# Kernel optimization log

Hardware: AMD Instinct MI355X
Metric: run time of the kernel (lower is better)

The kernel has to match this reference:

```python
import jax, jax.numpy as jnp
import numpy as np

N = 50000        # nodes
E = 1600000      # edges (before self loops)
IN = 128         # in_channels
HID = 32         # hidden_channels
HEADS = 4
OUT = 16         # out_channels
B = 512          # graphs in batch
NEG_SLOPE = 0.2  # PyG GATConv default


def _uniform(key, shape, fan_in):
    s = 1.0 / np.sqrt(fan_in)
    return jax.random.uniform(key, shape, jnp.float32, -s, s)


def setup_inputs() -> dict:
    key = jax.random.key(0)
    ks = jax.random.split(key, 12)
    x = jax.random.normal(ks[0], (N, IN), jnp.float32)
    edge_index = jax.random.randint(ks[1], (2, E), 0, N, dtype=jnp.int64)
    batch = jnp.sort(jax.random.randint(ks[2], (N,), 0, B, dtype=jnp.int64))
    return {
        "x": x,
        "edge_index": edge_index,
        "batch": batch,
        "W1": _uniform(ks[3], (IN, HEADS * HID), IN),
        "att_src": _uniform(ks[4], (HEADS, HID), HID),
        "att_dst": _uniform(ks[5], (HEADS, HID), HID),
        "b1": jnp.zeros((HEADS * HID,), jnp.float32),
        "lin1_w": _uniform(ks[6], (HEADS * HID, HID), HEADS * HID),
        "lin1_b": _uniform(ks[7], (HID,), HEADS * HID),
        "lin2_w": _uniform(ks[8], (HID, OUT), HID),
        "lin2_b": _uniform(ks[9], (OUT,), HID),
    }


def _gat_conv(x, src, dst, W1, att_src, att_dst, b1):
    # h: [N, H, C]
    h = (x @ W1).reshape(N, HEADS, HID)
    a_s = (h * att_src).sum(-1)   # [N, H]
    a_d = (h * att_dst).sum(-1)   # [N, H]
    # per-edge attention logits [E', H]
    alpha = jax.nn.leaky_relu(a_s[src] + a_d[dst], negative_slope=NEG_SLOPE)
    # segment softmax over incoming edges of each destination node
    amax = jax.lax.stop_gradient(jax.ops.segment_max(alpha, dst, num_segments=N))
    ex = jnp.exp(alpha - amax[dst])
    den = jax.ops.segment_sum(ex, dst, num_segments=N)
    a = ex / (den[dst] + 1e-16)
    # weighted scatter-aggregate of source features: [N, H, C]
    out = jax.ops.segment_sum(h[src] * a[:, :, None], dst, num_segments=N)
    return out.reshape(N, HEADS * HID) + b1


def reference(x, edge_index, batch, W1, att_src, att_dst, b1, lin1_w, lin1_b, lin2_w, lin2_b):
    # add self loops (PyG GATConv default add_self_loops=True)
    loop = jnp.arange(N, dtype=edge_index.dtype)
    src = jnp.concatenate([edge_index[0], loop])
    dst = jnp.concatenate([edge_index[1], loop])
    # dropout layers are identity in eval mode
    xh = jax.nn.elu(_gat_conv(x, src, dst, W1, att_src, att_dst, b1))
    g = jax.ops.segment_sum(xh, batch, num_segments=B)  # global_add_pool -> [B, H*C]
    g = g @ lin1_w + lin1_b
    return g @ lin2_w + lin2_b
```

## Files before the change

kernel.cpp:

```cpp
#include <hip/hip_runtime.h>
#include <hip/hip_bf16.h>
#include <hip/hip_fp16.h>

#define N_NODES 50000
#define E_EDGES 1600000
#define IN_CH 128
#define HID 32
#define HEADS 4
#define HC (HEADS * HID)
#define OUT_CH 16
#define B_GRAPHS 512
#define NEG_SLOPE 0.2f
#define CAP 96
#define NB 512
#define BNODES 98
#define PCAP 3584
#define ACHUNK 4096
#define APART 391
#define ROWS_PB 64
#define GEMM_BLOCKS 782
#define TOT_BLOCKS 1173

__device__ __forceinline__ unsigned short f2bf(float f) {
    unsigned int u = __float_as_uint(f);
    unsigned int r = (u + 0x7FFFu + ((u >> 16) & 1u)) >> 16;
    return (unsigned short)r;
}

__device__ __forceinline__ float lrelu_exp(float v) {
    v = v > 0.f ? v : NEG_SLOPE * v;
    return __expf(v);
}

__global__ __launch_bounds__(256) void k_fused(const float* __restrict__ x,
                                               const float* __restrict__ W1,
                                               const float* __restrict__ att_src,
                                               const float* __restrict__ att_dst,
                                               const int* __restrict__ ei,
                                               unsigned short* __restrict__ hb,
                                               float* __restrict__ a_s,
                                               float* __restrict__ a_d,
                                               int* __restrict__ gcur,
                                               unsigned int* __restrict__ ebuf,
                                               float* __restrict__ g) {
    __shared__ float smem[12288];
    const int t = threadIdx.x;
    const int bI = blockIdx.x;

    if (bI % 3 == 0) {
        const int ablk = bI / 3;
        int* scnt = (int*)smem;
        int* sbase = scnt + 4 * NB;
        const int wv = t >> 6;
        const int e0 = ablk * ACHUNK;
        int e1 = e0 + ACHUNK; if (e1 > E_EDGES) e1 = E_EDGES;
        for (int i = t; i < 4 * NB; i += 256) scnt[i] = 0;
        __syncthreads();
        const int* __restrict__ dstp = ei + E_EDGES;
        for (int e = e0 + t; e < e1; e += 256) {
            int d = dstp[e];
            atomicAdd(&scnt[wv * NB + d / BNODES], 1);
        }
        __syncthreads();
        for (int i = t; i < NB; i += 256) {
            int c0 = scnt[0 * NB + i], c1 = scnt[1 * NB + i];
            int c2 = scnt[2 * NB + i], c3 = scnt[3 * NB + i];
            int base = atomicAdd(&gcur[i], c0 + c1 + c2 + c3);
            sbase[0 * NB + i] = base;
            sbase[1 * NB + i] = base + c0;
            sbase[2 * NB + i] = base + c0 + c1;
            sbase[3 * NB + i] = base + c0 + c1 + c2;
            scnt[0 * NB + i] = 0; scnt[1 * NB + i] = 0;
            scnt[2 * NB + i] = 0; scnt[3 * NB + i] = 0;
        }
        __syncthreads();
        for (int e = e0 + t; e < e1; e += 256) {
            int d = dstp[e];
            int s = ei[e];
            int b = d / BNODES;
            int dl = d - b * BNODES;
            int pos = sbase[wv * NB + b] + atomicAdd(&scnt[wv * NB + b], 1);
            if (pos < PCAP)
                ebuf[(size_t)b * PCAP + pos] = ((unsigned int)dl << 16) | (unsigned int)s;
        }
        return;
    }

    float* sX = smem;
    float* sW = smem + 8192;
    const int bid = bI - bI / 3 - 1;
    const int n0 = bid * ROWS_PB;

    int gt = bid * 256 + t;
    if (gt < B_GRAPHS * HC) g[gt] = 0.f;

    for (int i = t; i < ROWS_PB * 32; i += 256) {
        int r = i >> 5, c4 = i & 31;
        int n = n0 + r;
        float4 v = (n < N_NODES) ? ((const float4*)x)[(size_t)n * 32 + c4]
                                 : make_float4(0.f, 0.f, 0.f, 0.f);
        ((float4*)sX)[i] = v;
    }

    float acc[8][4];
#pragma unroll
    for (int j = 0; j < 8; j++)
#pragma unroll
        for (int c = 0; c < 4; c++) acc[j][c] = 0.f;

    const int tx = t & 31;
    const int ty = t >> 5;

    for (int kb = 0; kb < 4; kb++) {
        __syncthreads();
        for (int i = t; i < 32 * 32; i += 256) {
            ((float4*)sW)[i] =
                ((const float4*)W1)[(size_t)(kb * 32 + (i >> 5)) * 32 + (i & 31)];
        }
        __syncthreads();
#pragma unroll
        for (int kk = 0; kk < 32; kk += 4) {
            float4 w0 = *(float4*)&sW[(kk + 0) * 128 + tx * 4];
            float4 w1 = *(float4*)&sW[(kk + 1) * 128 + tx * 4];
            float4 w2 = *(float4*)&sW[(kk + 2) * 128 + tx * 4];
            float4 w3 = *(float4*)&sW[(kk + 3) * 128 + tx * 4];
#pragma unroll
            for (int j = 0; j < 8; j++) {
                float4 xv = *(float4*)&sX[(ty * 8 + j) * 128 + kb * 32 + kk];
                acc[j][0] += xv.x * w0.x + xv.y * w1.x + xv.z * w2.x + xv.w * w3.x;
                acc[j][1] += xv.x * w0.y + xv.y * w1.y + xv.z * w2.y + xv.w * w3.y;
                acc[j][2] += xv.x * w0.z + xv.y * w1.z + xv.z * w2.z + xv.w * w3.z;
                acc[j][3] += xv.x * w0.w + xv.y * w1.w + xv.z * w2.w + xv.w * w3.w;
            }
        }
    }

#pragma unroll
    for (int j = 0; j < 8; j++) {
        int n = n0 + ty * 8 + j;
        if (n < N_NODES) {
            ushort4 o;
            o.x = f2bf(acc[j][0]); o.y = f2bf(acc[j][1]);
            o.z = f2bf(acc[j][2]); o.w = f2bf(acc[j][3]);
            *(ushort4*)&hb[(size_t)n * HC + tx * 4] = o;
        }
    }

    __syncthreads();
    float* sH = smem;
#pragma unroll
    for (int j = 0; j < 8; j++) {
        float* row = &sH[(ty * 8 + j) * 129 + tx * 4];
        row[0] = acc[j][0]; row[1] = acc[j][1];
        row[2] = acc[j][2]; row[3] = acc[j][3];
    }
    __syncthreads();
    if (t < 128) {
        int r = t & 63;
        int n = n0 + r;
        const float* __restrict__ av = (t < 64) ? att_src : att_dst;
        float s0 = 0.f, s1 = 0.f, s2 = 0.f, s3 = 0.f;
#pragma unroll 4
        for (int j = 0; j < 32; j++) {
            const float* row = &sH[r * 129 + j];
            s0 += row[0]  * av[j];
            s1 += row[32] * av[32 + j];
            s2 += row[64] * av[64 + j];
            s3 += row[96] * av[96 + j];
        }
        if (n < N_NODES) {
            float* dst = (t < 64) ? a_s : a_d;
            *(float4*)(dst + (size_t)n * 4) = make_float4(s0, s1, s2, s3);
        }
    }
}

#define NPW 7
__global__ __launch_bounds__(1024) void k_aggB(const unsigned int* __restrict__ ebuf,
                                               const int* __restrict__ gcur,
                                               const float* __restrict__ a_s,
                                               const float* __restrict__ a_d,
                                               const unsigned short* __restrict__ hb,
                                               const float* __restrict__ b1,
                                               const int* __restrict__ batch,
                                               float* __restrict__ g) {
    __shared__ unsigned short sbuf[BNODES * CAP];
    __shared__ int scnt[BNODES];
    __shared__ float sWt[16][4][97];
    const int t = threadIdx.x;
    const int b = blockIdx.x;
    const int dbase = b * BNODES;

    for (int i = t; i < BNODES; i += 1024) {
        int d = dbase + i;
        scnt[i] = (d < N_NODES) ? 1 : 0;
        sbuf[i * CAP] = (unsigned short)d;
    }
    __syncthreads();
    int m = gcur[b]; if (m > PCAP) m = PCAP;
    for (int i = t; i < m; i += 1024) {
        unsigned int p = ebuf[(size_t)b * PCAP + i];
        int dl = p >> 16;
        int s = p & 0xFFFFu;
        int c = atomicAdd(&scnt[dl], 1);
        if (c < CAP) sbuf[dl * CAP + c] = (unsigned short)s;
    }
    __syncthreads();

    const int wv = t >> 6;
    const int l = t & 63;
    const int head = l >> 4;
    const int c0 = 2 * l;
    int nl0 = wv * NPW;
    if (nl0 >= BNODES) return;
    int nl1 = nl0 + NPW; if (nl1 > BNODES) nl1 = BNODES;
    int gn0 = dbase + nl0;
    if (gn0 >= N_NODES) return;
    int gn1 = dbase + nl1; if (gn1 > N_NODES) gn1 = N_NODES;
    const float2 bias = *(const float2*)(b1 + c0);
    float pool0 = 0.f, pool1 = 0.f;
    int cur = batch[gn0];
    for (int n = gn0; n < gn1; n++) {
        int bb = batch[n];
        if (bb != cur) {
            atomicAdd(&g[(size_t)cur * HC + c0], pool0);
            atomicAdd(&g[(size_t)cur * HC + c0 + 1], pool1);
            pool0 = pool1 = 0.f;
            cur = bb;
        }
        int nl = n - dbase;
        int c = scnt[nl]; if (c > CAP) c = CAP;
        float4 ad = *(const float4*)(a_d + (size_t)n * 4);
        const unsigned short* __restrict__ srow = &sbuf[nl * CAP];
        for (int i = l; i < c; i += 64) {
            int s = srow[i];
            float4 as = *(const float4*)(a_s + (size_t)s * 4);
            sWt[wv][0][i] = lrelu_exp(as.x + ad.x);
            sWt[wv][1][i] = lrelu_exp(as.y + ad.y);
            sWt[wv][2][i] = lrelu_exp(as.z + ad.z);
            sWt[wv][3][i] = lrelu_exp(as.w + ad.w);
        }
        __asm__ volatile("" ::: "memory");
        const float* __restrict__ wrow = &sWt[wv][head][0];
        float acc0 = 0.f, acc1 = 0.f, dsum = 0.f;
        int i = 0;
        for (; i + 8 <= c; i += 8) {
            unsigned int u[8];
            float w[8];
#pragma unroll
            for (int q = 0; q < 8; q++) {
                int sq = srow[i + q];
                w[q] = wrow[i + q];
                u[q] = *(const unsigned int*)(hb + (size_t)sq * HC + c0);
            }
#pragma unroll
            for (int q = 0; q < 8; q++) {
                dsum += w[q];
                acc0 += w[q] * __uint_as_float(u[q] << 16);
                acc1 += w[q] * __uint_as_float(u[q] & 0xFFFF0000u);
            }
        }
        for (; i < c; i++) {
            int s0 = srow[i];
            float w0 = wrow[i];
            unsigned int u0 = *(const unsigned int*)(hb + (size_t)s0 * HC + c0);
            dsum += w0;
            acc0 += w0 * __uint_as_float(u0 << 16);
            acc1 += w0 * __uint_as_float(u0 & 0xFFFF0000u);
        }
        __asm__ volatile("" ::: "memory");
        float inv = 1.f / (dsum + 1e-16f);
        float v0 = acc0 * inv + bias.x; v0 = v0 > 0.f ? v0 : (__expf(v0) - 1.f);
        float v1 = acc1 * inv + bias.y; v1 = v1 > 0.f ? v1 : (__expf(v1) - 1.f);
        pool0 += v0;
        pool1 += v1;
    }
    atomicAdd(&g[(size_t)cur * HC + c0], pool0);
    atomicAdd(&g[(size_t)cur * HC + c0 + 1], pool1);
}

__global__ __launch_bounds__(64) void k_mlp(const float* __restrict__ g,
                                            const float* __restrict__ w1,
                                            const float* __restrict__ bb1,
                                            const float* __restrict__ w2,
                                            const float* __restrict__ bb2,
                                            float* __restrict__ out) {
    __shared__ float sg[HC];
    __shared__ float st[HID];
    int b = blockIdx.x;
    int t = threadIdx.x;
    sg[t]      = g[(size_t)b * HC + t];
    sg[t + 64] = g[(size_t)b * HC + 64 + t];
    __syncthreads();
    if (t < HID) {
        float acc = bb1[t];
#pragma unroll 8
        for (int k = 0; k < HC; k++) acc += sg[k] * w1[(size_t)k * HID + t];
        st[t] = acc;
    }
    __syncthreads();
    if (t < OUT_CH) {
        float acc = bb2[t];
#pragma unroll
        for (int k = 0; k < HID; k++) acc += st[k] * w2[(size_t)k * OUT_CH + t];
        out[(size_t)b * OUT_CH + t] = acc;
    }
}

extern "C" void kernel_launch(void* const* d_in, const int* in_sizes, int n_in,
                              void* d_out, int out_size, void* d_ws, size_t ws_size,
                              hipStream_t stream) {
    const float* x       = (const float*)d_in[0];
    const int*   ei      = (const int*)d_in[1];
    const int*   batch   = (const int*)d_in[2];
    const float* W1      = (const float*)d_in[3];
    const float* att_src = (const float*)d_in[4];
    const float* att_dst = (const float*)d_in[5];
    const float* b1      = (const float*)d_in[6];
    const float* lin1_w  = (const float*)d_in[7];
    const float* lin1_b  = (const float*)d_in[8];
    const float* lin2_w  = (const float*)d_in[9];
    const float* lin2_b  = (const float*)d_in[10];
    float* out = (float*)d_out;

    float* ws = (float*)d_ws;
    unsigned short* hb   = (unsigned short*)ws;
    float*  a_s      = ws + 3200000;
    float*  a_d      = ws + 3400000;
    unsigned int* ebuf = (unsigned int*)(ws + 3600000);
    int*    gcur     = (int*)(ws + 5435008);
    float*  g        = ws + 5436000;

    hipMemsetAsync(gcur, 0, NB * sizeof(int), stream);

    k_fused<<<TOT_BLOCKS, 256, 0, stream>>>(
        x, W1, att_src, att_dst, ei, hb, a_s, a_d, gcur, ebuf, g);
    k_aggB<<<NB, 1024, 0, stream>>>(ebuf, gcur, a_s, a_d, hb, b1, batch, g);
    k_mlp<<<B_GRAPHS, 64, 0, stream>>>(g, lin1_w, lin1_b, lin2_w, lin2_b, out);
}
```

Before: 207.9 us.

## Read GEMM operands directly from global memory and compute attention logits with shuffles

The node-projection GEMM in the fused kernel no longer stages x rows and W1 tiles through shared memory. Each thread now loads float4s straight from global memory and cache, which removes the staging loops and barriers. The per-node attention dot products are computed from the register accumulators with wave shuffles instead of a shared-memory transpose. Shared memory shrinks to 16 KB and launch bounds request 4 blocks per CU for higher occupancy, but global load traffic per block rises because x and W1 elements are no longer reused from LDS.

```diff
diff --git a/kernel.cpp b/kernel.cpp
--- a/kernel.cpp
+++ b/kernel.cpp
@@ -32,18 +32,18 @@
     return __expf(v);
 }
 
-__global__ __launch_bounds__(256) void k_fused(const float* __restrict__ x,
-                                               const float* __restrict__ W1,
-                                               const float* __restrict__ att_src,
-                                               const float* __restrict__ att_dst,
-                                               const int* __restrict__ ei,
-                                               unsigned short* __restrict__ hb,
-                                               float* __restrict__ a_s,
-                                               float* __restrict__ a_d,
-                                               int* __restrict__ gcur,
-                                               unsigned int* __restrict__ ebuf,
-                                               float* __restrict__ g) {
-    __shared__ float smem[12288];
+__global__ __launch_bounds__(256, 4) void k_fused(const float* __restrict__ x,
+                                                  const float* __restrict__ W1,
+                                                  const float* __restrict__ att_src,
+                                                  const float* __restrict__ att_dst,
+                                                  const int* __restrict__ ei,
+                                                  unsigned short* __restrict__ hb,
+                                                  float* __restrict__ a_s,
+                                                  float* __restrict__ a_d,
+                                                  int* __restrict__ gcur,
+                                                  unsigned int* __restrict__ ebuf,
+                                                  float* __restrict__ g) {
+    __shared__ float smem[4096];
     const int t = threadIdx.x;
     const int bI = blockIdx.x;
 
@@ -86,52 +86,42 @@
         return;
     }
 
-    float* sX = smem;
-    float* sW = smem + 8192;
     const int bid = bI - bI / 3 - 1;
     const int n0 = bid * ROWS_PB;
 
     int gt = bid * 256 + t;
     if (gt < B_GRAPHS * HC) g[gt] = 0.f;
 
-    for (int i = t; i < ROWS_PB * 32; i += 256) {
-        int r = i >> 5, c4 = i & 31;
-        int n = n0 + r;
-        float4 v = (n < N_NODES) ? ((const float4*)x)[(size_t)n * 32 + c4]
-                                 : make_float4(0.f, 0.f, 0.f, 0.f);
-        ((float4*)sX)[i] = v;
-    }
-
-    float acc[8][4];
-#pragma unroll
-    for (int j = 0; j < 8; j++)
-#pragma unroll
-        for (int c = 0; c < 4; c++) acc[j][c] = 0.f;
-
     const int tx = t & 31;
     const int ty = t >> 5;
 
-    for (int kb = 0; kb < 4; kb++) {
-        __syncthreads();
-        for (int i = t; i < 32 * 32; i += 256) {
-            ((float4*)sW)[i] =
-                ((const float4*)W1)[(size_t)(kb * 32 + (i >> 5)) * 32 + (i & 31)];
-        }
-        __syncthreads();
-#pragma unroll
-        for (int kk = 0; kk < 32; kk += 4) {
-            float4 w0 = *(float4*)&sW[(kk + 0) * 128 + tx * 4];
-            float4 w1 = *(float4*)&sW[(kk + 1) * 128 + tx * 4];
-            float4 w2 = *(float4*)&sW[(kk + 2) * 128 + tx * 4];
-            float4 w3 = *(float4*)&sW[(kk + 3) * 128 + tx * 4];
-#pragma unroll
-            for (int j = 0; j < 8; j++) {
-                float4 xv = *(float4*)&sX[(ty * 8 + j) * 128 + kb * 32 + kk];
-                acc[j][0] += xv.x * w0.x + xv.y * w1.x + xv.z * w2.x + xv.w * w3.x;
-                acc[j][1] += xv.x * w0.y + xv.y * w1.y + xv.z * w2.y + xv.w * w3.y;
-                acc[j][2] += xv.x * w0.z + xv.y * w1.z + xv.z * w2.z + xv.w * w3.z;
-                acc[j][3] += xv.x * w0.w + xv.y * w1.w + xv.z * w2.w + xv.w * w3.w;
-            }
+    const float* xb[8];
+#pragma unroll
+    for (int j = 0; j < 8; j++) {
+        int n = n0 + ty * 8 + j;
+        xb[j] = x + (size_t)(n < N_NODES ? n : 0) * IN_CH;
+    }
+    const float* wb = W1 + tx * 4;
+
+    float acc[8][4];
+#pragma unroll
+    for (int j = 0; j < 8; j++)
+#pragma unroll
+        for (int c = 0; c < 4; c++) acc[j][c] = 0.f;
+
+#pragma unroll 4
+    for (int kk = 0; kk < 128; kk += 4) {
+        float4 w0 = *(const float4*)(wb + (size_t)(kk + 0) * HC);
+        float4 w1 = *(const float4*)(wb + (size_t)(kk + 1) * HC);
+        float4 w2 = *(const float4*)(wb + (size_t)(kk + 2) * HC);
+        float4 w3 = *(const float4*)(wb + (size_t)(kk + 3) * HC);
+#pragma unroll
+        for (int j = 0; j < 8; j++) {
+            float4 xv = *(const float4*)(xb[j] + kk);
+            acc[j][0] += xv.x * w0.x + xv.y * w1.x + xv.z * w2.x + xv.w * w3.x;
+            acc[j][1] += xv.x * w0.y + xv.y * w1.y + xv.z * w2.y + xv.w * w3.y;
+            acc[j][2] += xv.x * w0.z + xv.y * w1.z + xv.z * w2.z + xv.w * w3.z;
+            acc[j][3] += xv.x * w0.w + xv.y * w1.w + xv.z * w2.w + xv.w * w3.w;
         }
     }
 
@@ -146,31 +136,21 @@
         }
     }
 
-    __syncthreads();
-    float* sH = smem;
+    float4 asv = ((const float4*)att_src)[tx];
+    float4 adv = ((const float4*)att_dst)[tx];
+    const int head = tx >> 3;
 #pragma unroll
     for (int j = 0; j < 8; j++) {
-        float* row = &sH[(ty * 8 + j) * 129 + tx * 4];
-        row[0] = acc[j][0]; row[1] = acc[j][1];
-        row[2] = acc[j][2]; row[3] = acc[j][3];
-    }
-    __syncthreads();
-    if (t < 128) {
-        int r = t & 63;
-        int n = n0 + r;
-        const float* __restrict__ av = (t < 64) ? att_src : att_dst;
-        float s0 = 0.f, s1 = 0.f, s2 = 0.f, s3 = 0.f;
-#pragma unroll 4
-        for (int j = 0; j < 32; j++) {
-            const float* row = &sH[r * 129 + j];
-            s0 += row[0]  * av[j];
-            s1 += row[32] * av[32 + j];
-            s2 += row[64] * av[64 + j];
-            s3 += row[96] * av[96 + j];
-        }
-        if (n < N_NODES) {
-            float* dst = (t < 64) ? a_s : a_d;
-            *(float4*)(dst + (size_t)n * 4) = make_float4(s0, s1, s2, s3);
+        float sp = acc[j][0] * asv.x + acc[j][1] * asv.y +
+                   acc[j][2] * asv.z + acc[j][3] * asv.w;
+        float dp = acc[j][0] * adv.x + acc[j][1] * adv.y +
+                   acc[j][2] * adv.z + acc[j][3] * adv.w;
+        sp += __shfl_xor(sp, 1); sp += __shfl_xor(sp, 2); sp += __shfl_xor(sp, 4);
+        dp += __shfl_xor(dp, 1); dp += __shfl_xor(dp, 2); dp += __shfl_xor(dp, 4);
+        int n = n0 + ty * 8 + j;
+        if ((tx & 7) == 0 && n < N_NODES) {
+            a_s[(size_t)n * 4 + head] = sp;
+            a_d[(size_t)n * 4 + head] = dp;
         }
     }
 }
```

Result: slower. 423.3 us (+103.7%).

## Use split-bf16 MFMA for the x@W1 projection with pre-transposed weights

Applied to the files above, without the earlier changes.

Replaces the FP32 FMA tiled GEMM for x@W1 with bf16 MFMA instructions. Both x and W1 are split into high and low bf16 parts and three products are summed to keep near-FP32 accuracy. A new small prep kernel transposes and splits W1 (and clears gcur instead of a memset). The x tile is stored in a swizzled LDS layout, which also cuts shared memory use. PCAP shrinks so the per-bucket edge buffer ends before the new weight workspace region.

```diff
diff --git a/kernel.cpp b/kernel.cpp
--- a/kernel.cpp
+++ b/kernel.cpp
@@ -14,13 +14,16 @@
 #define CAP 96
 #define NB 512
 #define BNODES 98
-#define PCAP 3584
+#define PCAP 3552
 #define ACHUNK 4096
 #define APART 391
 #define ROWS_PB 64
 #define GEMM_BLOCKS 782
 #define TOT_BLOCKS 1173
 
+typedef short bfrag __attribute__((ext_vector_type(8)));
+typedef float facc  __attribute__((ext_vector_type(4)));
+
 __device__ __forceinline__ unsigned short f2bf(float f) {
     unsigned int u = __float_as_uint(f);
     unsigned int r = (u + 0x7FFFu + ((u >> 16) & 1u)) >> 16;
@@ -32,8 +35,23 @@
     return __expf(v);
 }
 
+__global__ __launch_bounds__(256) void k_prep(const float* __restrict__ W1,
+                                              unsigned short* __restrict__ whiT,
+                                              unsigned short* __restrict__ wloT,
+                                              int* __restrict__ gcur) {
+    int tid = blockIdx.x * 256 + threadIdx.x;
+    if (tid < NB) gcur[tid] = 0;
+    int k = tid >> 7, n = tid & 127;
+    float v = W1[tid];
+    unsigned int u = __float_as_uint(v);
+    float lo_f = v - __uint_as_float(u & 0xFFFF0000u);
+    whiT[n * 128 + k] = (unsigned short)(u >> 16);
+    wloT[n * 128 + k] = f2bf(lo_f);
+}
+
 __global__ __launch_bounds__(256) void k_fused(const float* __restrict__ x,
-                                               const float* __restrict__ W1,
+                                               const unsigned short* __restrict__ whiT,
+                                               const unsigned short* __restrict__ wloT,
                                                const float* __restrict__ att_src,
                                                const float* __restrict__ att_dst,
                                                const int* __restrict__ ei,
@@ -43,7 +61,7 @@
                                                int* __restrict__ gcur,
                                                unsigned int* __restrict__ ebuf,
                                                float* __restrict__ g) {
-    __shared__ float smem[12288];
+    __shared__ float smem[8256];
     const int t = threadIdx.x;
     const int bI = blockIdx.x;
 
@@ -86,73 +104,89 @@
         return;
     }
 
-    float* sX = smem;
-    float* sW = smem + 8192;
+    unsigned short* sxh = (unsigned short*)smem;
+    unsigned short* sxl = sxh + 64 * 128;
     const int bid = bI - bI / 3 - 1;
     const int n0 = bid * ROWS_PB;
 
     int gt = bid * 256 + t;
     if (gt < B_GRAPHS * HC) g[gt] = 0.f;
 
-    for (int i = t; i < ROWS_PB * 32; i += 256) {
+    for (int it = 0; it < 8; it++) {
+        int i = t + it * 256;
         int r = i >> 5, c4 = i & 31;
         int n = n0 + r;
         float4 v = (n < N_NODES) ? ((const float4*)x)[(size_t)n * 32 + c4]
                                  : make_float4(0.f, 0.f, 0.f, 0.f);
-        ((float4*)sX)[i] = v;
-    }
-
-    float acc[8][4];
-#pragma unroll
-    for (int j = 0; j < 8; j++)
-#pragma unroll
-        for (int c = 0; c < 4; c++) acc[j][c] = 0.f;
-
-    const int tx = t & 31;
-    const int ty = t >> 5;
-
-    for (int kb = 0; kb < 4; kb++) {
-        __syncthreads();
-        for (int i = t; i < 32 * 32; i += 256) {
-            ((float4*)sW)[i] =
-                ((const float4*)W1)[(size_t)(kb * 32 + (i >> 5)) * 32 + (i & 31)];
-        }
-        __syncthreads();
-#pragma unroll
-        for (int kk = 0; kk < 32; kk += 4) {
-            float4 w0 = *(float4*)&sW[(kk + 0) * 128 + tx * 4];
-            float4 w1 = *(float4*)&sW[(kk + 1) * 128 + tx * 4];
-            float4 w2 = *(float4*)&sW[(kk + 2) * 128 + tx * 4];
-            float4 w3 = *(float4*)&sW[(kk + 3) * 128 + tx * 4];
-#pragma unroll
-            for (int j = 0; j < 8; j++) {
-                float4 xv = *(float4*)&sX[(ty * 8 + j) * 128 + kb * 32 + kk];
-                acc[j][0] += xv.x * w0.x + xv.y * w1.x + xv.z * w2.x + xv.w * w3.x;
-                acc[j][1] += xv.x * w0.y + xv.y * w1.y + xv.z * w2.y + xv.w * w3.y;
-                acc[j][2] += xv.x * w0.z + xv.y * w1.z + xv.z * w2.z + xv.w * w3.z;
-                acc[j][3] += xv.x * w0.w + xv.y * w1.w + xv.z * w2.w + xv.w * w3.w;
+        unsigned int ux = __float_as_uint(v.x), uy = __float_as_uint(v.y);
+        unsigned int uz = __float_as_uint(v.z), uw = __float_as_uint(v.w);
+        unsigned int uh0 = (ux >> 16) | (uy & 0xFFFF0000u);
+        unsigned int uh1 = (uz >> 16) | (uw & 0xFFFF0000u);
+        float lx = v.x - __uint_as_float(ux & 0xFFFF0000u);
+        float ly = v.y - __uint_as_float(uy & 0xFFFF0000u);
+        float lz = v.z - __uint_as_float(uz & 0xFFFF0000u);
+        float lw = v.w - __uint_as_float(uw & 0xFFFF0000u);
+        unsigned int ul0 = (unsigned int)f2bf(lx) | ((unsigned int)f2bf(ly) << 16);
+        unsigned int ul1 = (unsigned int)f2bf(lz) | ((unsigned int)f2bf(lw) << 16);
+        int byo = r * 256 + (((c4 >> 1) ^ (r & 7)) << 4) + (c4 & 1) * 8;
+        *(uint2*)((char*)sxh + byo) = make_uint2(uh0, uh1);
+        *(uint2*)((char*)sxl + byo) = make_uint2(ul0, ul1);
+    }
+    __syncthreads();
+
+    const int wv = t >> 6, l = t & 63;
+    const int lm = l & 15, lk = l >> 4;
+    const int band = wv * 16;
+
+    bfrag ahi[4], alo[4];
+    {
+        int row = band + lm;
+#pragma unroll
+        for (int kc = 0; kc < 4; kc++) {
+            int sl = (kc * 4 + lk) ^ (row & 7);
+            ahi[kc] = *(const bfrag*)((const char*)sxh + row * 256 + sl * 16);
+            alo[kc] = *(const bfrag*)((const char*)sxl + row * 256 + sl * 16);
+        }
+    }
+
+    facc acc[8];
+#pragma unroll
+    for (int nt = 0; nt < 8; nt++) acc[nt] = (facc){0.f, 0.f, 0.f, 0.f};
+
+    {
+        const int cb = lm * 128 + lk * 8;
+#pragma unroll
+        for (int nt = 0; nt < 8; nt++) {
+            const unsigned short* bh = whiT + cb + nt * (16 * 128);
+            const unsigned short* bl = wloT + cb + nt * (16 * 128);
+#pragma unroll
+            for (int kc = 0; kc < 4; kc++) {
+                bfrag bhv = *(const bfrag*)(bh + kc * 32);
+                bfrag blv = *(const bfrag*)(bl + kc * 32);
+                acc[nt] = __builtin_amdgcn_mfma_f32_16x16x32_bf16(ahi[kc], bhv, acc[nt], 0, 0, 0);
+                acc[nt] = __builtin_amdgcn_mfma_f32_16x16x32_bf16(alo[kc], bhv, acc[nt], 0, 0, 0);
+                acc[nt] = __builtin_amdgcn_mfma_f32_16x16x32_bf16(ahi[kc], blv, acc[nt], 0, 0, 0);
             }
         }
     }
 
 #pragma unroll
-    for (int j = 0; j < 8; j++) {
-        int n = n0 + ty * 8 + j;
-        if (n < N_NODES) {
-            ushort4 o;
-            o.x = f2bf(acc[j][0]); o.y = f2bf(acc[j][1]);
-            o.z = f2bf(acc[j][2]); o.w = f2bf(acc[j][3]);
-            *(ushort4*)&hb[(size_t)n * HC + tx * 4] = o;
+    for (int nt = 0; nt < 8; nt++) {
+#pragma unroll
+        for (int r = 0; r < 4; r++) {
+            int n = n0 + band + lk * 4 + r;
+            if (n < N_NODES)
+                hb[(size_t)n * HC + nt * 16 + lm] = f2bf(acc[nt][r]);
         }
     }
 
     __syncthreads();
     float* sH = smem;
 #pragma unroll
-    for (int j = 0; j < 8; j++) {
-        float* row = &sH[(ty * 8 + j) * 129 + tx * 4];
-        row[0] = acc[j][0]; row[1] = acc[j][1];
-        row[2] = acc[j][2]; row[3] = acc[j][3];
+    for (int nt = 0; nt < 8; nt++) {
+#pragma unroll
+        for (int r = 0; r < 4; r++)
+            sH[(band + lk * 4 + r) * 129 + nt * 16 + lm] = acc[nt][r];
     }
     __syncthreads();
     if (t < 128) {
@@ -328,13 +362,14 @@
     float*  a_s      = ws + 3200000;
     float*  a_d      = ws + 3400000;
     unsigned int* ebuf = (unsigned int*)(ws + 3600000);
+    unsigned short* whiT = (unsigned short*)(ws + 5418624);
+    unsigned short* wloT = (unsigned short*)(ws + 5426816);
     int*    gcur     = (int*)(ws + 5435008);
     float*  g        = ws + 5436000;
 
-    hipMemsetAsync(gcur, 0, NB * sizeof(int), stream);
-
+    k_prep<<<64, 256, 0, stream>>>(W1, whiT, wloT, gcur);
     k_fused<<<TOT_BLOCKS, 256, 0, stream>>>(
-        x, W1, att_src, att_dst, ei, hb, a_s, a_d, gcur, ebuf, g);
+        x, whiT, wloT, att_src, att_dst, ei, hb, a_s, a_d, gcur, ebuf, g);
     k_aggB<<<NB, 1024, 0, stream>>>(ebuf, gcur, a_s, a_d, hb, b1, batch, g);
     k_mlp<<<B_GRAPHS, 64, 0, stream>>>(g, lin1_w, lin1_b, lin2_w, lin2_b, out);
 }
```

New measurement: 211.3 us. No clear change (+1.7%).
